# Kernel tuning notes

Measured on AMD Instinct MI355X. Metric: run time of the kernel, lower is better.

Reference implementation:

```python
import jax, jax.numpy as jnp
import numpy as np

N_NODES = 50000
N_EDGES = 800000


def setup_inputs() -> dict:
    key = jax.random.key(0)
    ks = jax.random.split(key, 8)
    x = jax.random.normal(ks[0], (N_NODES, 128), dtype=jnp.float32)
    edge_index = jax.random.randint(ks[1], (2, N_EDGES), 0, N_NODES, dtype=jnp.int64)
    # Glorot-ish scaled weights (GCNConv uses glorot init)
    W1 = jax.random.normal(ks[2], (128, 128), dtype=jnp.float32) * 0.08
    W2 = jax.random.normal(ks[3], (128, 128), dtype=jnp.float32) * 0.08
    W3 = jax.random.normal(ks[4], (128, 64), dtype=jnp.float32) * 0.08
    b1 = jnp.zeros((128,), jnp.float32)
    b2 = jnp.zeros((128,), jnp.float32)
    b3 = jnp.zeros((64,), jnp.float32)
    return {"x": x, "W1": W1, "b1": b1, "W2": W2, "b2": b2,
            "W3": W3, "b3": b3, "edge_index": edge_index}


def _gcn_layer(x, W, b, src, dst, norm, n):
    # GCNConv: out = D^{-1/2} (A+I) D^{-1/2} (x W) + b
    h = x @ W                                   # [N, F_out]
    msg = h[src] * norm[:, None]                # gather + scale per edge
    agg = jax.ops.segment_sum(msg, dst, num_segments=n)  # scatter-add
    return agg + b


def reference(x, W1, b1, W2, b2, W3, b3, edge_index):
    n = x.shape[0]
    loops = jnp.arange(n, dtype=edge_index.dtype)
    src = jnp.concatenate([edge_index[0], loops])  # add self-loops (PyG default)
    dst = jnp.concatenate([edge_index[1], loops])
    # symmetric normalization from in-degree (incl. self-loops)
    deg = jax.ops.segment_sum(jnp.ones_like(dst, dtype=x.dtype), dst, num_segments=n)
    dis = jnp.where(deg > 0, jax.lax.rsqrt(deg), 0.0)
    norm = dis[src] * dis[dst]                   # [E+N]

    h = jax.nn.relu(_gcn_layer(x, W1, b1, src, dst, norm, n))
    # dropout(p=0.5) is identity in eval mode
    h = jax.nn.relu(_gcn_layer(h, W2, b2, src, dst, norm, n))
    h = _gcn_layer(h, W3, b3, src, dst, norm, n)
    return jax.nn.log_softmax(h, axis=1)
```

## Files before the change

kernel.cpp:

```cpp
#include <hip/hip_runtime.h>
#include <hip/hip_bf16.h>
#include <cstdint>

typedef unsigned int uint32;
typedef __attribute__((ext_vector_type(8))) short short8;
typedef __attribute__((ext_vector_type(4))) float f32x4;

#define EPB 4096

__device__ inline unsigned short bf16r(float f) {
    uint32 u = __float_as_uint(f);
    u += 0x7fff + ((u >> 16) & 1);
    return (unsigned short)(u >> 16);
}
__device__ inline uint32 pack_bf16(float a, float b) {
    return (uint32)bf16r(a) | ((uint32)bf16r(b) << 16);
}
__device__ inline float bf_lo(uint32 w) { return __uint_as_float(w << 16); }
__device__ inline float bf_hi(uint32 w) { return __uint_as_float(w & 0xffff0000u); }


__global__ void k_init_i32(int* __restrict__ p, int n) {
    int i = blockIdx.x * blockDim.x + threadIdx.x;
    if (i < n) p[i] = 0;
}

__global__ __launch_bounds__(256) void k_bhist(const int* __restrict__ dstv,
                                               int* __restrict__ bhist, int e) {
    __shared__ int h[256];
    int t = threadIdx.x;
    h[t] = 0;
    __syncthreads();
    int b0 = blockIdx.x * EPB;
#pragma unroll
    for (int i = 0; i < EPB / 256; ++i) {
        int idx = b0 + i * 256 + t;
        if (idx < e) atomicAdd(&h[dstv[idx] >> 8], 1);
    }
    __syncthreads();
    if (h[t]) atomicAdd(&bhist[t], h[t]);
}

__global__ __launch_bounds__(256) void k_bscan(const int* __restrict__ bhist,
                                               int* __restrict__ bpre, int* __restrict__ bcur,
                                               int nb, int e, int* __restrict__ rp, int n) {
    __shared__ int s[256];
    int t = threadIdx.x;
    int v = (t < nb) ? bhist[t] : 0;
    s[t] = v;
    __syncthreads();
    for (int off = 1; off < 256; off <<= 1) {
        int a = (t >= off) ? s[t - off] : 0;
        __syncthreads();
        s[t] += a;
        __syncthreads();
    }
    if (t < nb) { bpre[t] = s[t] - v; bcur[t] = s[t] - v; }
    if (t == 0) { bpre[nb] = e; rp[n] = e; }
}

__global__ __launch_bounds__(256) void k_partition(const int* __restrict__ srcv,
                                                   const int* __restrict__ dstv,
                                                   int* __restrict__ bcur,
                                                   uint2* __restrict__ pairs, int e) {
    __shared__ int h[256], base[256], cur[256];
    int t = threadIdx.x;
    h[t] = 0; cur[t] = 0;
    __syncthreads();
    int s[EPB / 256], d[EPB / 256];
    int b0 = blockIdx.x * EPB;
#pragma unroll
    for (int i = 0; i < EPB / 256; ++i) {
        int idx = b0 + i * 256 + t;
        if (idx < e) {
            s[i] = srcv[idx]; d[i] = dstv[idx];
            atomicAdd(&h[d[i] >> 8], 1);
        } else d[i] = -1;
    }
    __syncthreads();
    if (h[t]) base[t] = atomicAdd(&bcur[t], h[t]);
    __syncthreads();
#pragma unroll
    for (int i = 0; i < EPB / 256; ++i) {
        if (d[i] >= 0) {
            int b = d[i] >> 8;
            int sl = atomicAdd(&cur[b], 1);
            pairs[base[b] + sl] = make_uint2((unsigned)s[i], (unsigned)d[i]);
        }
    }
}

__global__ __launch_bounds__(256) void k_bfinish(const uint2* __restrict__ pairs,
                                                 const int* __restrict__ bpre,
                                                 int* __restrict__ rp, float* __restrict__ dis,
                                                 int* __restrict__ col, int n) {
    __shared__ int c[256], sc[256], cur[256];
    int t = threadIdx.x;
    c[t] = 0; cur[t] = 0;
    __syncthreads();
    int wb = blockIdx.x << 8;
    int e0 = bpre[blockIdx.x], e1 = bpre[blockIdx.x + 1];
    for (int i = e0 + t; i < e1; i += 256) atomicAdd(&c[(int)pairs[i].y - wb], 1);
    __syncthreads();
    int own = c[t];
    sc[t] = own;
    __syncthreads();
    for (int off = 1; off < 256; off <<= 1) {
        int a = (t >= off) ? sc[t - off] : 0;
        __syncthreads();
        sc[t] += a;
        __syncthreads();
    }
    int base = bpre[blockIdx.x] + sc[t] - own;
    __syncthreads();
    sc[t] = base;
    int v = wb + t;
    if (v < n) { rp[v] = base; dis[v] = rsqrtf((float)(own + 1)); }
    __syncthreads();
    for (int i = e0 + t; i < e1; i += 256) {
        uint2 p = pairs[i];
        int bl = (int)p.y - wb;
        int sl = atomicAdd(&cur[bl], 1);
        col[sc[bl] + sl] = (int)p.x;
    }
}


__global__ __launch_bounds__(256) void k_wprep(const float* __restrict__ W1,
                                               const float* __restrict__ W2,
                                               const float* __restrict__ W3,
                                               unsigned short* __restrict__ Wt1,
                                               unsigned short* __restrict__ Wt2,
                                               unsigned short* __restrict__ Wt3) {
    const float* W = blockIdx.x == 0 ? W1 : (blockIdx.x == 1 ? W2 : W3);
    unsigned short* Wt = blockIdx.x == 0 ? Wt1 : (blockIdx.x == 1 ? Wt2 : Wt3);
    int F = blockIdx.x == 2 ? 64 : 128;
    for (int i = threadIdx.x; i < 128 * F; i += 256) {
        int k = i / F, c = i % F;
        Wt[c * 128 + k] = bf16r(W[i]);
    }
}


template <int FOUT, bool BF16IN>
__global__ __launch_bounds__(256) void k_gemm_mfma(
        const void* __restrict__ Xv, const unsigned short* __restrict__ Wt,
        const float* __restrict__ dis, unsigned short* __restrict__ Yb, int n) {
    constexpr int CT = FOUT / 16;
    int lane = threadIdx.x & 63;
    int wv = threadIdx.x >> 6;
    int r16 = lane & 15, kg = lane >> 4;
    int rowA = blockIdx.x * 64 + wv * 16 + r16;
    int ra = min(rowA, n - 1);
    short8 afr[4];
    if (BF16IN) {
        const unsigned short* Xb = (const unsigned short*)Xv;
#pragma unroll
        for (int ks = 0; ks < 4; ++ks)
            afr[ks] = *(const short8*)(Xb + (size_t)ra * 128 + ks * 32 + kg * 8);
    } else {
        const float* Xf = (const float*)Xv;
#pragma unroll
        for (int ks = 0; ks < 4; ++ks) {
            const float* p = Xf + (size_t)ra * 128 + ks * 32 + kg * 8;
            float4 f0 = *(const float4*)p;
            float4 f1 = *(const float4*)(p + 4);
            short8 a;
            a[0] = (short)bf16r(f0.x); a[1] = (short)bf16r(f0.y);
            a[2] = (short)bf16r(f0.z); a[3] = (short)bf16r(f0.w);
            a[4] = (short)bf16r(f1.x); a[5] = (short)bf16r(f1.y);
            a[6] = (short)bf16r(f1.z); a[7] = (short)bf16r(f1.w);
            afr[ks] = a;
        }
    }
    f32x4 acc[CT];
#pragma unroll
    for (int c = 0; c < CT; ++c) acc[c] = (f32x4){0.f, 0.f, 0.f, 0.f};
#pragma unroll
    for (int ks = 0; ks < 4; ++ks) {
#pragma unroll
        for (int c = 0; c < CT; ++c) {
            short8 b = *(const short8*)(Wt + (c * 16 + r16) * 128 + ks * 32 + kg * 8);
            acc[c] = __builtin_amdgcn_mfma_f32_16x16x32_bf16(afr[ks], b, acc[c], 0, 0, 0);
        }
    }
    int rbase = blockIdx.x * 64 + wv * 16 + kg * 4;
#pragma unroll
    for (int j = 0; j < 4; ++j) {
        int row = rbase + j;
        if (row < n) {
            float d = dis[row];
#pragma unroll
            for (int c = 0; c < CT; ++c)
                Yb[(size_t)row * FOUT + c * 16 + r16] = bf16r(acc[c][j] * d);
        }
    }
}


__global__ __launch_bounds__(256) void k_agg_relu128(
        const uint32* __restrict__ hb, const int* __restrict__ rp,
        const int* __restrict__ col, const float* __restrict__ dis,
        const float* __restrict__ bias, uint32* __restrict__ outb, int n) {
    int wid = threadIdx.x >> 6;
    int lane = threadIdx.x & 63;
    int v = blockIdx.x * 4 + wid;
    if (v >= n) return;
    uint32 mv = hb[(size_t)v * 64 + lane];
    float ax = bf_lo(mv), ay = bf_hi(mv);
    int s = __builtin_amdgcn_readfirstlane(rp[v]);
    int e = __builtin_amdgcn_readfirstlane(rp[v + 1]);
    int k = s;
    for (; k + 16 <= e; k += 16) {
        uint32 m[16];
#pragma unroll
        for (int j = 0; j < 16; ++j) {
            int u = col[k + j];
            m[j] = hb[(size_t)u * 64 + lane];
        }
#pragma unroll
        for (int j = 0; j < 16; ++j) { ax += bf_lo(m[j]); ay += bf_hi(m[j]); }
    }
    if (k + 8 <= e) {
        uint32 m[8];
#pragma unroll
        for (int j = 0; j < 8; ++j) m[j] = hb[(size_t)col[k + j] * 64 + lane];
#pragma unroll
        for (int j = 0; j < 8; ++j) { ax += bf_lo(m[j]); ay += bf_hi(m[j]); }
        k += 8;
    }
    if (k + 4 <= e) {
        uint32 m[4];
#pragma unroll
        for (int j = 0; j < 4; ++j) m[j] = hb[(size_t)col[k + j] * 64 + lane];
#pragma unroll
        for (int j = 0; j < 4; ++j) { ax += bf_lo(m[j]); ay += bf_hi(m[j]); }
        k += 4;
    }
    for (; k < e; ++k) {
        uint32 m = hb[(size_t)col[k] * 64 + lane];
        ax += bf_lo(m); ay += bf_hi(m);
    }
    float d = dis[v];
    float2 b = ((const float2*)bias)[lane];
    float ox = fmaxf(d * ax + b.x, 0.f);
    float oy = fmaxf(d * ay + b.y, 0.f);
    outb[(size_t)v * 64 + lane] = pack_bf16(ox, oy);
}

__global__ __launch_bounds__(256) void k_agg_lsm64(
        const unsigned short* __restrict__ hb, const int* __restrict__ rp,
        const int* __restrict__ col, const float* __restrict__ dis,
        const float* __restrict__ bias, float* __restrict__ out, int n) {
    int wid = threadIdx.x >> 6;
    int lane = threadIdx.x & 63;
    int v = blockIdx.x * 4 + wid;
    if (v >= n) return;
    float acc = __uint_as_float((uint32)hb[(size_t)v * 64 + lane] << 16);
    int s = __builtin_amdgcn_readfirstlane(rp[v]);
    int e = __builtin_amdgcn_readfirstlane(rp[v + 1]);
    int k = s;
    for (; k + 16 <= e; k += 16) {
        unsigned short m[16];
#pragma unroll
        for (int j = 0; j < 16; ++j) m[j] = hb[(size_t)col[k + j] * 64 + lane];
#pragma unroll
        for (int j = 0; j < 16; ++j) acc += __uint_as_float((uint32)m[j] << 16);
    }
    if (k + 8 <= e) {
        unsigned short m[8];
#pragma unroll
        for (int j = 0; j < 8; ++j) m[j] = hb[(size_t)col[k + j] * 64 + lane];
#pragma unroll
        for (int j = 0; j < 8; ++j) acc += __uint_as_float((uint32)m[j] << 16);
        k += 8;
    }
    for (; k < e; ++k) acc += __uint_as_float((uint32)hb[(size_t)col[k] * 64 + lane] << 16);
    float val = dis[v] * acc + bias[lane];
    float m = val;
    for (int off = 32; off; off >>= 1) m = fmaxf(m, __shfl_xor(m, off, 64));
    float ex = expf(val - m);
    float ss = ex;
    for (int off = 32; off; off >>= 1) ss += __shfl_xor(ss, off, 64);
    out[(size_t)v * 64 + lane] = val - m - logf(ss);
}


extern "C" void kernel_launch(void* const* d_in, const int* in_sizes, int n_in,
                              void* d_out, int out_size, void* d_ws, size_t ws_size,
                              hipStream_t stream) {
    const float* x  = (const float*)d_in[0];
    const float* W1 = (const float*)d_in[1];
    const float* b1 = (const float*)d_in[2];
    const float* W2 = (const float*)d_in[3];
    const float* b2 = (const float*)d_in[4];
    const float* W3 = (const float*)d_in[5];
    const float* b3 = (const float*)d_in[6];
    const int*   ei = (const int*)d_in[7];

    const int N = in_sizes[0] / 128;
    const int E = in_sizes[7] / 2;
    const int* srcv = ei;
    const int* dstv = ei + E;
    const int NB = (N + 255) >> 8;

    char* ws = (char*)d_ws;
    size_t off = 0;
    auto alloc = [&](size_t bytes) -> void* {
        void* p = ws + off;
        off += (bytes + 255) & ~(size_t)255;
        return p;
    };
    float*          dis   = (float*)alloc((size_t)N * 4);
    int*            rp    = (int*)alloc((size_t)(N + 1) * 4);
    int*            col   = (int*)alloc((size_t)E * 4);
    int*            bhist = (int*)alloc((size_t)(NB + 1) * 4);
    int*            bpre  = (int*)alloc((size_t)(NB + 1) * 4);
    int*            bcur  = (int*)alloc((size_t)(NB + 1) * 4);
    uint2*          pairs = (uint2*)alloc((size_t)E * 8);
    unsigned short* Wt1   = (unsigned short*)alloc(128 * 128 * 2);
    unsigned short* Wt2   = (unsigned short*)alloc(128 * 128 * 2);
    unsigned short* Wt3   = (unsigned short*)alloc(64 * 128 * 2);
    unsigned short* hsb   = (unsigned short*)alloc((size_t)N * 128 * 2);
    unsigned short* hbX   = (unsigned short*)alloc((size_t)N * 128 * 2);
    float*          outp  = (float*)d_out;

    const int tb = 256;
    const int nbE = (E + EPB - 1) / EPB;

    k_init_i32<<<(NB + tb - 1) / tb, tb, 0, stream>>>(bhist, NB);
    k_bhist<<<nbE, 256, 0, stream>>>(dstv, bhist, E);
    k_bscan<<<1, 256, 0, stream>>>(bhist, bpre, bcur, NB, E, rp, N);
    k_partition<<<nbE, 256, 0, stream>>>(srcv, dstv, bcur, pairs, E);
    k_bfinish<<<NB, 256, 0, stream>>>(pairs, bpre, rp, dis, col, N);
    k_wprep<<<3, 256, 0, stream>>>(W1, W2, W3, Wt1, Wt2, Wt3);

    int gblk = (N + 63) / 64;
    int ablk = (N + 3) / 4;
    k_gemm_mfma<128, false><<<gblk, 256, 0, stream>>>(x, Wt1, dis, hsb, N);
    k_agg_relu128<<<ablk, 256, 0, stream>>>((const uint32*)hsb, rp, col, dis, b1, (uint32*)hbX, N);
    k_gemm_mfma<128, true><<<gblk, 256, 0, stream>>>(hbX, Wt2, dis, hsb, N);
    k_agg_relu128<<<ablk, 256, 0, stream>>>((const uint32*)hsb, rp, col, dis, b2, (uint32*)hbX, N);
    k_gemm_mfma<64, true><<<gblk, 256, 0, stream>>>(hbX, Wt3, dis, hsb, N);
    k_agg_lsm64<<<ablk, 256, 0, stream>>>(hsb, rp, col, dis, b3, outp, N);
}
```

Before: 207.7 us.

## Pad CSR rows to multiples of 16 with a zero dummy node, drop tail loops

Each node's adjacency list is padded to a multiple of 16 entries, using an extra zeroed row at index N as the padding target. This lets the aggregation kernels run only full 16-wide unrolled gather loops with no 8/4/1 remainder branches, and row bounds are read as an int2 pair. The per-block histogram is written to a global array and reduced inside the scan, which removes the init kernel and global atomics. Weight prep and dummy-row zeroing are folded into the histogram launch to cut the launch count. The cost is wasted gathers on padding (about 7.5 extra entries per node on average, for roughly 16 real edges), a larger col buffer, and a serial per-thread loop in the scan.

```diff
diff --git a/kernel.cpp b/kernel.cpp
--- a/kernel.cpp
+++ b/kernel.cpp
@@ -3,15 +3,17 @@
 #include <cstdint>
 
 typedef unsigned int uint32;
+typedef unsigned short ushort;
 typedef __attribute__((ext_vector_type(8))) short short8;
 typedef __attribute__((ext_vector_type(4))) float f32x4;
 
 #define EPB 4096
-
-__device__ inline unsigned short bf16r(float f) {
+#define SLACK 3840
+
+__device__ inline ushort bf16r(float f) {
     uint32 u = __float_as_uint(f);
     u += 0x7fff + ((u >> 16) & 1);
-    return (unsigned short)(u >> 16);
+    return (ushort)(u >> 16);
 }
 __device__ inline uint32 pack_bf16(float a, float b) {
     return (uint32)bf16r(a) | ((uint32)bf16r(b) << 16);
@@ -20,33 +22,49 @@
 __device__ inline float bf_hi(uint32 w) { return __uint_as_float(w & 0xffff0000u); }
 
 
-__global__ void k_init_i32(int* __restrict__ p, int n) {
-    int i = blockIdx.x * blockDim.x + threadIdx.x;
-    if (i < n) p[i] = 0;
-}
-
-__global__ __launch_bounds__(256) void k_bhist(const int* __restrict__ dstv,
-                                               int* __restrict__ bhist, int e) {
+__global__ __launch_bounds__(256) void k_bhist_prep(
+        const int* __restrict__ dstv, int* __restrict__ hglob, int e, int nbE,
+        const float* __restrict__ W1, const float* __restrict__ W2, const float* __restrict__ W3,
+        ushort* __restrict__ Wt1, ushort* __restrict__ Wt2, ushort* __restrict__ Wt3,
+        ushort* __restrict__ hsb, ushort* __restrict__ hs3, int n) {
     __shared__ int h[256];
-    int t = threadIdx.x;
-    h[t] = 0;
-    __syncthreads();
-    int b0 = blockIdx.x * EPB;
-#pragma unroll
-    for (int i = 0; i < EPB / 256; ++i) {
-        int idx = b0 + i * 256 + t;
-        if (idx < e) atomicAdd(&h[dstv[idx] >> 8], 1);
-    }
-    __syncthreads();
-    if (h[t]) atomicAdd(&bhist[t], h[t]);
-}
-
-__global__ __launch_bounds__(256) void k_bscan(const int* __restrict__ bhist,
+    int bid = blockIdx.x, t = threadIdx.x;
+    if (bid < nbE) {
+        h[t] = 0;
+        __syncthreads();
+        int b0 = bid * EPB;
+#pragma unroll
+        for (int i = 0; i < EPB / 256; ++i) {
+            int idx = b0 + i * 256 + t;
+            if (idx < e) atomicAdd(&h[dstv[idx] >> 8], 1);
+        }
+        __syncthreads();
+        hglob[bid * 256 + t] = h[t];
+    } else {
+        int wb = bid - nbE;
+        if (wb < 3) {
+            const float* W = wb == 0 ? W1 : (wb == 1 ? W2 : W3);
+            ushort* Wt = wb == 0 ? Wt1 : (wb == 1 ? Wt2 : Wt3);
+            int F = wb == 2 ? 64 : 128;
+            for (int i = t; i < 128 * F; i += 256) {
+                int k = i / F, c = i % F;
+                Wt[c * 128 + k] = bf16r(W[i]);
+            }
+        } else {
+            if (t < 128) hsb[(size_t)n * 128 + t] = 0;
+            if (t < 64)  hs3[(size_t)n * 64 + t] = 0;
+        }
+    }
+}
+
+
+__global__ __launch_bounds__(256) void k_bscan(const int* __restrict__ hglob, int nbE,
                                                int* __restrict__ bpre, int* __restrict__ bcur,
-                                               int nb, int e, int* __restrict__ rp, int n) {
+                                               int nb, int e) {
     __shared__ int s[256];
     int t = threadIdx.x;
-    int v = (t < nb) ? bhist[t] : 0;
+    int v = 0;
+    for (int b = 0; b < nbE; ++b) v += hglob[b * 256 + t];
     s[t] = v;
     __syncthreads();
     for (int off = 1; off < 256; off <<= 1) {
@@ -56,8 +74,9 @@
         __syncthreads();
     }
     if (t < nb) { bpre[t] = s[t] - v; bcur[t] = s[t] - v; }
-    if (t == 0) { bpre[nb] = e; rp[n] = e; }
-}
+    if (t == 0) bpre[nb] = e;
+}
+
 
 __global__ __launch_bounds__(256) void k_partition(const int* __restrict__ srcv,
                                                    const int* __restrict__ dstv,
@@ -90,9 +109,10 @@
     }
 }
 
+
 __global__ __launch_bounds__(256) void k_bfinish(const uint2* __restrict__ pairs,
                                                  const int* __restrict__ bpre,
-                                                 int* __restrict__ rp, float* __restrict__ dis,
+                                                 int2* __restrict__ rps, float* __restrict__ dis,
                                                  int* __restrict__ col, int n) {
     __shared__ int c[256], sc[256], cur[256];
     int t = threadIdx.x;
@@ -103,7 +123,8 @@
     for (int i = e0 + t; i < e1; i += 256) atomicAdd(&c[(int)pairs[i].y - wb], 1);
     __syncthreads();
     int own = c[t];
-    sc[t] = own;
+    int pad = (own + 15) & ~15;
+    sc[t] = pad;
     __syncthreads();
     for (int off = 1; off < 256; off <<= 1) {
         int a = (t >= off) ? sc[t - off] : 0;
@@ -111,11 +132,14 @@
         sc[t] += a;
         __syncthreads();
     }
-    int base = bpre[blockIdx.x] + sc[t] - own;
-    __syncthreads();
-    sc[t] = base;
+    int start = bpre[blockIdx.x] + blockIdx.x * SLACK + sc[t] - pad;
+    __syncthreads();
+    sc[t] = start;
     int v = wb + t;
-    if (v < n) { rp[v] = base; dis[v] = rsqrtf((float)(own + 1)); }
+    if (v < n) {
+        rps[v] = make_int2(start, start + pad);
+        dis[v] = rsqrtf((float)(own + 1));
+    }
     __syncthreads();
     for (int i = e0 + t; i < e1; i += 256) {
         uint2 p = pairs[i];
@@ -123,29 +147,15 @@
         int sl = atomicAdd(&cur[bl], 1);
         col[sc[bl] + sl] = (int)p.x;
     }
-}
-
-
-__global__ __launch_bounds__(256) void k_wprep(const float* __restrict__ W1,
-                                               const float* __restrict__ W2,
-                                               const float* __restrict__ W3,
-                                               unsigned short* __restrict__ Wt1,
-                                               unsigned short* __restrict__ Wt2,
-                                               unsigned short* __restrict__ Wt3) {
-    const float* W = blockIdx.x == 0 ? W1 : (blockIdx.x == 1 ? W2 : W3);
-    unsigned short* Wt = blockIdx.x == 0 ? Wt1 : (blockIdx.x == 1 ? Wt2 : Wt3);
-    int F = blockIdx.x == 2 ? 64 : 128;
-    for (int i = threadIdx.x; i < 128 * F; i += 256) {
-        int k = i / F, c = i % F;
-        Wt[c * 128 + k] = bf16r(W[i]);
-    }
+    __syncthreads();
+    for (int i = own; i < pad; ++i) col[start + i] = n;
 }
 
 
 template <int FOUT, bool BF16IN>
 __global__ __launch_bounds__(256) void k_gemm_mfma(
-        const void* __restrict__ Xv, const unsigned short* __restrict__ Wt,
-        const float* __restrict__ dis, unsigned short* __restrict__ Yb, int n) {
+        const void* __restrict__ Xv, const ushort* __restrict__ Wt,
+        const float* __restrict__ dis, ushort* __restrict__ Yb, int n) {
     constexpr int CT = FOUT / 16;
     int lane = threadIdx.x & 63;
     int wv = threadIdx.x >> 6;
@@ -154,7 +164,7 @@
     int ra = min(rowA, n - 1);
     short8 afr[4];
     if (BF16IN) {
-        const unsigned short* Xb = (const unsigned short*)Xv;
+        const ushort* Xb = (const ushort*)Xv;
 #pragma unroll
         for (int ks = 0; ks < 4; ++ks)
             afr[ks] = *(const short8*)(Xb + (size_t)ra * 128 + ks * 32 + kg * 8);
@@ -199,7 +209,7 @@
 
 
 __global__ __launch_bounds__(256) void k_agg_relu128(
-        const uint32* __restrict__ hb, const int* __restrict__ rp,
+        const uint32* __restrict__ hb, const int2* __restrict__ rps,
         const int* __restrict__ col, const float* __restrict__ dis,
         const float* __restrict__ bias, uint32* __restrict__ outb, int n) {
     int wid = threadIdx.x >> 6;
@@ -208,10 +218,10 @@
     if (v >= n) return;
     uint32 mv = hb[(size_t)v * 64 + lane];
     float ax = bf_lo(mv), ay = bf_hi(mv);
-    int s = __builtin_amdgcn_readfirstlane(rp[v]);
-    int e = __builtin_amdgcn_readfirstlane(rp[v + 1]);
-    int k = s;
-    for (; k + 16 <= e; k += 16) {
+    int2 se = rps[v];
+    int s = __builtin_amdgcn_readfirstlane(se.x);
+    int e = __builtin_amdgcn_readfirstlane(se.y);
+    for (int k = s; k < e; k += 16) {
         uint32 m[16];
 #pragma unroll
         for (int j = 0; j < 16; ++j) {
@@ -220,26 +230,6 @@
         }
 #pragma unroll
         for (int j = 0; j < 16; ++j) { ax += bf_lo(m[j]); ay += bf_hi(m[j]); }
-    }
-    if (k + 8 <= e) {
-        uint32 m[8];
-#pragma unroll
-        for (int j = 0; j < 8; ++j) m[j] = hb[(size_t)col[k + j] * 64 + lane];
-#pragma unroll
-        for (int j = 0; j < 8; ++j) { ax += bf_lo(m[j]); ay += bf_hi(m[j]); }
-        k += 8;
-    }
-    if (k + 4 <= e) {
-        uint32 m[4];
-#pragma unroll
-        for (int j = 0; j < 4; ++j) m[j] = hb[(size_t)col[k + j] * 64 + lane];
-#pragma unroll
-        for (int j = 0; j < 4; ++j) { ax += bf_lo(m[j]); ay += bf_hi(m[j]); }
-        k += 4;
-    }
-    for (; k < e; ++k) {
-        uint32 m = hb[(size_t)col[k] * 64 + lane];
-        ax += bf_lo(m); ay += bf_hi(m);
     }
     float d = dis[v];
     float2 b = ((const float2*)bias)[lane];
@@ -249,7 +239,7 @@
 }
 
 __global__ __launch_bounds__(256) void k_agg_lsm64(
-        const unsigned short* __restrict__ hb, const int* __restrict__ rp,
+        const ushort* __restrict__ hb, const int2* __restrict__ rps,
         const int* __restrict__ col, const float* __restrict__ dis,
         const float* __restrict__ bias, float* __restrict__ out, int n) {
     int wid = threadIdx.x >> 6;
@@ -257,25 +247,16 @@
     int v = blockIdx.x * 4 + wid;
     if (v >= n) return;
     float acc = __uint_as_float((uint32)hb[(size_t)v * 64 + lane] << 16);
-    int s = __builtin_amdgcn_readfirstlane(rp[v]);
-    int e = __builtin_amdgcn_readfirstlane(rp[v + 1]);
-    int k = s;
-    for (; k + 16 <= e; k += 16) {
-        unsigned short m[16];
+    int2 se = rps[v];
+    int s = __builtin_amdgcn_readfirstlane(se.x);
+    int e = __builtin_amdgcn_readfirstlane(se.y);
+    for (int k = s; k < e; k += 16) {
+        ushort m[16];
 #pragma unroll
         for (int j = 0; j < 16; ++j) m[j] = hb[(size_t)col[k + j] * 64 + lane];
 #pragma unroll
         for (int j = 0; j < 16; ++j) acc += __uint_as_float((uint32)m[j] << 16);
     }
-    if (k + 8 <= e) {
-        unsigned short m[8];
-#pragma unroll
-        for (int j = 0; j < 8; ++j) m[j] = hb[(size_t)col[k + j] * 64 + lane];
-#pragma unroll
-        for (int j = 0; j < 8; ++j) acc += __uint_as_float((uint32)m[j] << 16);
-        k += 8;
-    }
-    for (; k < e; ++k) acc += __uint_as_float((uint32)hb[(size_t)col[k] * 64 + lane] << 16);
     float val = dis[v] * acc + bias[lane];
     float m = val;
     for (int off = 32; off; off >>= 1) m = fmaxf(m, __shfl_xor(m, off, 64));
@@ -302,7 +283,8 @@
     const int E = in_sizes[7] / 2;
     const int* srcv = ei;
     const int* dstv = ei + E;
-    const int NB = (N + 255) >> 8;
+    const int NB  = (N + 255) >> 8;
+    const int nbE = (E + EPB - 1) / EPB;
 
     char* ws = (char*)d_ws;
     size_t off = 0;
@@ -311,36 +293,33 @@
         off += (bytes + 255) & ~(size_t)255;
         return p;
     };
-    float*          dis   = (float*)alloc((size_t)N * 4);
-    int*            rp    = (int*)alloc((size_t)(N + 1) * 4);
-    int*            col   = (int*)alloc((size_t)E * 4);
-    int*            bhist = (int*)alloc((size_t)(NB + 1) * 4);
-    int*            bpre  = (int*)alloc((size_t)(NB + 1) * 4);
-    int*            bcur  = (int*)alloc((size_t)(NB + 1) * 4);
-    uint2*          pairs = (uint2*)alloc((size_t)E * 8);
-    unsigned short* Wt1   = (unsigned short*)alloc(128 * 128 * 2);
-    unsigned short* Wt2   = (unsigned short*)alloc(128 * 128 * 2);
-    unsigned short* Wt3   = (unsigned short*)alloc(64 * 128 * 2);
-    unsigned short* hsb   = (unsigned short*)alloc((size_t)N * 128 * 2);
-    unsigned short* hbX   = (unsigned short*)alloc((size_t)N * 128 * 2);
-    float*          outp  = (float*)d_out;
-
-    const int tb = 256;
-    const int nbE = (E + EPB - 1) / EPB;
-
-    k_init_i32<<<(NB + tb - 1) / tb, tb, 0, stream>>>(bhist, NB);
-    k_bhist<<<nbE, 256, 0, stream>>>(dstv, bhist, E);
-    k_bscan<<<1, 256, 0, stream>>>(bhist, bpre, bcur, NB, E, rp, N);
+    float*  dis   = (float*)alloc((size_t)N * 4);
+    int2*   rps   = (int2*)alloc((size_t)N * 8);
+    int*    col   = (int*)alloc(((size_t)E + (size_t)NB * SLACK + 16) * 4);
+    int*    hglob = (int*)alloc((size_t)nbE * 256 * 4);
+    int*    bpre  = (int*)alloc((size_t)(NB + 1) * 4);
+    int*    bcur  = (int*)alloc((size_t)(NB + 1) * 4);
+    uint2*  pairs = (uint2*)alloc((size_t)E * 8);
+    ushort* Wt1   = (ushort*)alloc(128 * 128 * 2);
+    ushort* Wt2   = (ushort*)alloc(128 * 128 * 2);
+    ushort* Wt3   = (ushort*)alloc(64 * 128 * 2);
+    ushort* hsb   = (ushort*)alloc((size_t)(N + 1) * 128 * 2);
+    ushort* hbX   = (ushort*)alloc((size_t)N * 128 * 2);
+    ushort* hs3   = (ushort*)alloc((size_t)(N + 1) * 64 * 2);
+    float*  outp  = (float*)d_out;
+
+    k_bhist_prep<<<nbE + 4, 256, 0, stream>>>(dstv, hglob, E, nbE,
+                                              W1, W2, W3, Wt1, Wt2, Wt3, hsb, hs3, N);
+    k_bscan<<<1, 256, 0, stream>>>(hglob, nbE, bpre, bcur, NB, E);
     k_partition<<<nbE, 256, 0, stream>>>(srcv, dstv, bcur, pairs, E);
-    k_bfinish<<<NB, 256, 0, stream>>>(pairs, bpre, rp, dis, col, N);
-    k_wprep<<<3, 256, 0, stream>>>(W1, W2, W3, Wt1, Wt2, Wt3);
+    k_bfinish<<<NB, 256, 0, stream>>>(pairs, bpre, rps, dis, col, N);
 
     int gblk = (N + 63) / 64;
     int ablk = (N + 3) / 4;
     k_gemm_mfma<128, false><<<gblk, 256, 0, stream>>>(x, Wt1, dis, hsb, N);
-    k_agg_relu128<<<ablk, 256, 0, stream>>>((const uint32*)hsb, rp, col, dis, b1, (uint32*)hbX, N);
+    k_agg_relu128<<<ablk, 256, 0, stream>>>((const uint32*)hsb, rps, col, dis, b1, (uint32*)hbX, N);
     k_gemm_mfma<128, true><<<gblk, 256, 0, stream>>>(hbX, Wt2, dis, hsb, N);
-    k_agg_relu128<<<ablk, 256, 0, stream>>>((const uint32*)hsb, rp, col, dis, b2, (uint32*)hbX, N);
-    k_gemm_mfma<64, true><<<gblk, 256, 0, stream>>>(hbX, Wt3, dis, hsb, N);
-    k_agg_lsm64<<<ablk, 256, 0, stream>>>(hsb, rp, col, dis, b3, outp, N);
-}
+    k_agg_relu128<<<ablk, 256, 0, stream>>>((const uint32*)hsb, rps, col, dis, b2, (uint32*)hbX, N);
+    k_gemm_mfma<64, true><<<gblk, 256, 0, stream>>>(hbX, Wt3, dis, hs3, N);
+    k_agg_lsm64<<<ablk, 256, 0, stream>>>(hs3, rps, col, dis, b3, outp, N);
+}
```

Measured after the change: 214.8 us. 1.03x slower.
